# Performance work log

Measured on AMD Instinct MI355X. Metric: run time of the kernel, lower is better.

Reference implementation:

```python
import jax, jax.numpy as jnp
import numpy as np

EPS = 1e-6          # VN leaky-relu denominator eps (vn_layers.py)
NEG_SLOPE = 0.2     # VNLinearLeakyReLU default negative_slope
K = 3               # pointops.interpolation default k
DIST_EPS = 1e-8     # interpolation inverse-distance eps


def vn_linear_leakyrelu(x, w_feat, w_dir):
    # x: [B, Cin, 3, N]; w_*: [Cout, Cin]  (bias-free Linears over channel dim)
    p = jnp.einsum('oc,bcvn->bovn', w_feat, x)
    d = jnp.einsum('oc,bcvn->bovn', w_dir, x)
    dot = jnp.sum(p * d, axis=2, keepdims=True)          # [B,Cout,1,N]
    d2 = jnp.sum(d * d, axis=2, keepdims=True)
    mask = (dot >= 0).astype(x.dtype)
    proj = p - (dot / (d2 + EPS)) * d                    # reflect negative part onto plane perp to d
    return NEG_SLOPE * p + (1.0 - NEG_SLOPE) * (mask * p + (1.0 - mask) * proj)


def interpolation(p2, p1, feat, b, n2, n1):
    # p2: [b*n2,3] coarse coords, p1: [b*n1,3] fine coords, feat: [C,3,b*n2]
    # k-NN inverse-squared-distance interpolation, segment-local per cloud.
    C = feat.shape[0]
    p2b = p2.reshape(b, n2, 3)
    p1b = p1.reshape(b, n1, 3)
    featb = feat.reshape(C * 3, b, n2).transpose(1, 2, 0)  # [b, n2, C*3]

    def per_batch(q, s, f):
        d2 = jnp.sum((q[:, None, :] - s[None, :, :]) ** 2, axis=-1)  # [n1,n2]
        neg_d2, idx = jax.lax.top_k(-d2, K)                          # k smallest sq-dists
        w = 1.0 / (-neg_d2 + DIST_EPS)
        w = w / jnp.sum(w, axis=1, keepdims=True)                    # [n1,K]
        return jnp.einsum('nk,nkc->nc', w, f[idx])                   # [n1, C*3]

    out = jax.vmap(per_batch)(p1b, p2b, featb)                       # [b, n1, C*3]
    return out.reshape(b, n1, C, 3).transpose(2, 3, 0, 1).reshape(C, 3, b * n1)


def setup_inputs() -> dict:
    key = jax.random.key(0)
    ks = jax.random.split(key, 8)
    b, n1, n2 = 4, 16384, 4096
    in_planes, out_planes = 128, 64
    p1 = jax.random.uniform(ks[0], (b * n1, 3), dtype=jnp.float32)
    p2 = jax.random.uniform(ks[1], (b * n2, 3), dtype=jnp.float32)
    x1 = jax.random.normal(ks[2], (1, out_planes, 3, b * n1), dtype=jnp.float32)
    x2 = jax.random.normal(ks[3], (1, in_planes, 3, b * n2), dtype=jnp.float32)
    o1 = (jnp.arange(1, b + 1, dtype=jnp.int32)) * n1   # cumulative offsets
    o2 = (jnp.arange(1, b + 1, dtype=jnp.int32)) * n2
    s1 = 1.0 / np.sqrt(out_planes)
    s2 = 1.0 / np.sqrt(in_planes)
    w1_feat = jax.random.uniform(ks[4], (out_planes, out_planes), jnp.float32, -s1, s1)
    w1_dir = jax.random.uniform(ks[5], (out_planes, out_planes), jnp.float32, -s1, s1)
    w2_feat = jax.random.uniform(ks[6], (out_planes, in_planes), jnp.float32, -s2, s2)
    w2_dir = jax.random.uniform(ks[7], (out_planes, in_planes), jnp.float32, -s2, s2)
    return {"p1": p1, "x1": x1, "o1": o1, "p2": p2, "x2": x2, "o2": o2,
            "w1_feat": w1_feat, "w1_dir": w1_dir, "w2_feat": w2_feat, "w2_dir": w2_dir}


def reference(p1, x1, o1, p2, x2, o2, w1_feat, w1_dir, w2_feat, w2_dir):
    b = o1.shape[0]
    n1 = x1.shape[-1] // b
    n2 = x2.shape[-1] // b
    y1 = vn_linear_leakyrelu(x1, w1_feat, w1_dir)            # [1,Cout,3,N1]
    y2 = vn_linear_leakyrelu(x2, w2_feat, w2_dir)[0]         # squeeze(0) -> [Cout,3,N2]
    up = interpolation(p2, p1, y2, b, n2, n1)                # [Cout,3,N1]
    return y1 + up
```

## Files before the change

kernel.cpp:

```cpp
#include <hip/hip_runtime.h>

#define N1T 65536
#define N2T 16384
#define COUT 64
#define CH 192
#define GRD 8
#define HCELL 0.125f

typedef unsigned short bhalf;
typedef __attribute__((ext_vector_type(8))) short short8;
typedef __attribute__((ext_vector_type(4))) float f32x4;

__device__ __forceinline__ bhalf f2bf(float f) {
    unsigned u = __float_as_uint(f);
    return (bhalf)((u + 0x7FFFu + ((u >> 16) & 1u)) >> 16);
}
__device__ __forceinline__ float bf2f(bhalf h) {
    return __uint_as_float(((unsigned)h) << 16);
}

__global__ __launch_bounds__(256) void prep_kernel(
    const float* __restrict__ w1f, const float* __restrict__ w1d,
    const float* __restrict__ w2f, const float* __restrict__ w2d,
    bhalf* __restrict__ o1fh, bhalf* __restrict__ o1fl,
    bhalf* __restrict__ o1dh, bhalf* __restrict__ o1dl,
    bhalf* __restrict__ o2fh, bhalf* __restrict__ o2fl,
    bhalf* __restrict__ o2dh, bhalf* __restrict__ o2dl,
    int* __restrict__ zp) {
    if (blockIdx.x < 32) {
        const int i = blockIdx.x * 256 + threadIdx.x;
        if (i < 4096) {
            const float a = w1f[i]; const bhalf ah = f2bf(a);
            o1fh[i] = ah; o1fl[i] = f2bf(a - bf2f(ah));
            const float b = w1d[i]; const bhalf bh = f2bf(b);
            o1dh[i] = bh; o1dl[i] = f2bf(b - bf2f(bh));
        }
        const float a = w2f[i]; const bhalf ah = f2bf(a);
        o2fh[i] = ah; o2fl[i] = f2bf(a - bf2f(ah));
        const float b = w2d[i]; const bhalf bh = f2bf(b);
        o2dh[i] = bh; o2dl[i] = f2bf(b - bf2f(bh));
    } else {
        const int i = (blockIdx.x - 32) * 256 + threadIdx.x;
        if (i < 4096) zp[i] = 0;
    }
}

template<int CIN, int N, bool CM, int NT>
__global__ __launch_bounds__(512) void vn_mfma_kernel(
    const float* __restrict__ x,
    const bhalf* __restrict__ wfh, const bhalf* __restrict__ wfl,
    const bhalf* __restrict__ wdh, const bhalf* __restrict__ wdl,
    const int*   __restrict__ idxs,
    const float* __restrict__ wts,
    const float* __restrict__ y2t,
    float* __restrict__ out)
{
    constexpr int ROWS = CIN * 3;
    constexpr int LDSC = CIN * 3 + 8;
    constexpr int NB   = (NT > 1) ? 2 : 1;
    constexpr int NLD  = ROWS * 8 / 512;
    __shared__ __align__(16) bhalf xs_h[NB][32][LDSC];
    __shared__ __align__(16) bhalf xs_l[NB][32][LDSC];

    const int tid  = threadIdx.x;
    const int lane = tid & 63;
    const int wave = tid >> 6;
    const int r16  = lane & 15;
    const int hh   = lane >> 4;
    const int ot   = wave & 3;
    const int sW   = wave >> 2;
    const int pt   = sW * 16 + r16;
    const int tile0 = blockIdx.x * NT;

    int gk[NT][3]; float gw[NT][3];
    if constexpr (CM) {
#pragma unroll
        for (int t = 0; t < NT; ++t) {
            const int n = (tile0 + t) * 32 + pt;
#pragma unroll
            for (int r = 0; r < 3; ++r) {
                gk[t][r] = idxs[r * N1T + n];
                gw[t][r] = wts[r * N1T + n];
            }
        }
    }

    const int wofs = (ot * 16 + r16) * CIN + hh * 8;
    const bhalf* __restrict__ pfh = wfh + wofs;
    const bhalf* __restrict__ pfl = wfl + wofs;
    const bhalf* __restrict__ pdh = wdh + wofs;
    const bhalf* __restrict__ pdl = wdl + wofs;
    const int hs = ((hh ^ (r16 >> 2)) & 3) * 8;

    auto LOADT = [&](float4 (&st)[NLD], int t) {
#pragma unroll
        for (int r = 0; r < NLD; ++r) {
            const int i4 = r * 512 + tid;
            const int row = i4 >> 3, p4 = i4 & 7;
            st[r] = *(const float4*)&x[(size_t)row * N + (size_t)(tile0 + t) * 32 + p4 * 4];
        }
    };
    auto WRITET = [&](const float4 (&st)[NLD], int b) {
#pragma unroll
        for (int r = 0; r < NLD; ++r) {
            const int i4 = r * 512 + tid;
            const int row = i4 >> 3, p4 = i4 & 7;
            const int c = row / 3, vv = row - c * 3;
            const int colS = (vv * CIN + c) ^ ((p4 & 3) << 3);
            const float vals[4] = {st[r].x, st[r].y, st[r].z, st[r].w};
#pragma unroll
            for (int j = 0; j < 4; ++j) {
                const bhalf h = f2bf(vals[j]);
                xs_h[b][p4*4+j][colS] = h;
                xs_l[b][p4*4+j][colS] = f2bf(vals[j] - bf2f(h));
            }
        }
    };
    auto COMPUTET = [&](int t, int b, const int (&gkt)[3], const float (&gwt)[3]) {
        const f32x4 zero = {0.f, 0.f, 0.f, 0.f};
        f32x4 accP[3], accD[3];
#pragma unroll
        for (int v = 0; v < 3; ++v) { accP[v] = zero; accD[v] = zero; }
#pragma unroll
        for (int k = 0; k < CIN / 32; ++k) {
            const short8 afh = *(const short8*)(pfh + k * 32);
            const short8 afl = *(const short8*)(pfl + k * 32);
            const short8 adh = *(const short8*)(pdh + k * 32);
            const short8 adl = *(const short8*)(pdl + k * 32);
#pragma unroll
            for (int v = 0; v < 3; ++v) {
                const short8 bh = *(const short8*)&xs_h[b][pt][v * CIN + k * 32 + hs];
                const short8 bl = *(const short8*)&xs_l[b][pt][v * CIN + k * 32 + hs];
                accP[v] = __builtin_amdgcn_mfma_f32_16x16x32_bf16(afh, bh, accP[v], 0, 0, 0);
                accP[v] = __builtin_amdgcn_mfma_f32_16x16x32_bf16(afl, bh, accP[v], 0, 0, 0);
                accP[v] = __builtin_amdgcn_mfma_f32_16x16x32_bf16(afh, bl, accP[v], 0, 0, 0);
                accD[v] = __builtin_amdgcn_mfma_f32_16x16x32_bf16(adh, bh, accD[v], 0, 0, 0);
                accD[v] = __builtin_amdgcn_mfma_f32_16x16x32_bf16(adl, bh, accD[v], 0, 0, 0);
                accD[v] = __builtin_amdgcn_mfma_f32_16x16x32_bf16(adh, bl, accD[v], 0, 0, 0);
            }
        }
        float rr[12];
#pragma unroll
        for (int reg = 0; reg < 4; ++reg) {
            const float p0 = accP[0][reg], p1 = accP[1][reg], p2 = accP[2][reg];
            const float q0 = accD[0][reg], q1 = accD[1][reg], q2 = accD[2][reg];
            const float dot = p0*q0 + p1*q1 + p2*q2;
            const float dd  = q0*q0 + q1*q1 + q2*q2;
            const float coef = (dot < 0.f) ? (0.8f * dot / (dd + 1e-6f)) : 0.f;
            rr[reg*3+0] = p0 - coef * q0;
            rr[reg*3+1] = p1 - coef * q1;
            rr[reg*3+2] = p2 - coef * q2;
        }
        const int n = (tile0 + t) * 32 + pt;
        if constexpr (!CM) {
            float* op = out + (size_t)n * CH + ot * 48 + hh * 12;
            *(float4*)&op[0] = make_float4(rr[0], rr[1], rr[2],  rr[3]);
            *(float4*)&op[4] = make_float4(rr[4], rr[5], rr[6],  rr[7]);
            *(float4*)&op[8] = make_float4(rr[8], rr[9], rr[10], rr[11]);
        } else {
            const int chb = ot * 48 + hh * 12;
            const float* __restrict__ r0 = y2t + (size_t)gkt[0] * CH + chb;
            const float* __restrict__ r1 = y2t + (size_t)gkt[1] * CH + chb;
            const float* __restrict__ r2 = y2t + (size_t)gkt[2] * CH + chb;
            const float w0 = gwt[0], w1 = gwt[1], w2 = gwt[2];
            float4 a0[3], a1[3], a2[3];
#pragma unroll
            for (int q = 0; q < 3; ++q) {
                a0[q] = *(const float4*)&r0[q * 4];
                a1[q] = *(const float4*)&r1[q * 4];
                a2[q] = *(const float4*)&r2[q * 4];
            }
#pragma unroll
            for (int q = 0; q < 3; ++q) {
                const float u0 = w0*a0[q].x + w1*a1[q].x + w2*a2[q].x;
                const float u1 = w0*a0[q].y + w1*a1[q].y + w2*a2[q].y;
                const float u2 = w0*a0[q].z + w1*a1[q].z + w2*a2[q].z;
                const float u3 = w0*a0[q].w + w1*a1[q].w + w2*a2[q].w;
                out[(size_t)(chb + q*4 + 0) * N + n] = rr[q*4+0] + u0;
                out[(size_t)(chb + q*4 + 1) * N + n] = rr[q*4+1] + u1;
                out[(size_t)(chb + q*4 + 2) * N + n] = rr[q*4+2] + u2;
                out[(size_t)(chb + q*4 + 3) * N + n] = rr[q*4+3] + u3;
            }
        }
    };

    float4 stA[NLD], stB[NLD];
    LOADT(stA, 0);
    WRITET(stA, 0);
    if constexpr (NT == 2) {
        LOADT(stB, 1);
        __syncthreads();
        COMPUTET(0, 0, gk[0], gw[0]);
        WRITET(stB, 1);
        __syncthreads();
        COMPUTET(1, 1, gk[1], gw[1]);
    } else {
        __syncthreads();
        COMPUTET(0, 0, gk[0], gw[0]);
    }
}

#define KNN_INSERT(d2, j)                                        \
    {                                                            \
        const bool c0 = (d2) < b0;                               \
        const bool c1 = (d2) < b1;                               \
        const bool c2 = (d2) < b2v;                              \
        const float nb2 = c2 ? (c1 ? b1 : (d2)) : b2v;           \
        const int   ni2 = c2 ? (c1 ? i1 : (j))  : i2;            \
        const float nb1 = c1 ? (c0 ? b0 : (d2)) : b1;            \
        const int   ni1 = c1 ? (c0 ? i0 : (j))  : i1;            \
        b0 = c0 ? (d2) : b0;  i0 = c0 ? (j) : i0;                \
        b1 = nb1; i1 = ni1; b2v = nb2; i2 = ni2;                 \
    }

__device__ __forceinline__ int cell_of(float x, float y, float z) {
    int cx = (int)(x * (float)GRD); cx = cx < 0 ? 0 : (cx > GRD-1 ? GRD-1 : cx);
    int cy = (int)(y * (float)GRD); cy = cy < 0 ? 0 : (cy > GRD-1 ? GRD-1 : cy);
    int cz = (int)(z * (float)GRD); cz = cz < 0 ? 0 : (cz > GRD-1 ? GRD-1 : cz);
    return (cz << 6) | (cy << 3) | cx;
}

__global__ __launch_bounds__(256) void bin_count_kernel(
    const float* __restrict__ p2, int* __restrict__ counts) {
    const int i = blockIdx.x * 256 + threadIdx.x;
    const float x = p2[i*3+0], y = p2[i*3+1], z = p2[i*3+2];
    const int cell = ((i >> 12) << 9) | cell_of(x, y, z);
    atomicAdd(&counts[cell], 1);
}

__global__ __launch_bounds__(256) void scan_kernel(
    const int* __restrict__ counts, int* __restrict__ off) {
    __shared__ int buf[2][256];
    const int t = threadIdx.x;
    int v[8]; int s = 0;
#pragma unroll
    for (int j = 0; j < 8; ++j) { const int tmp = counts[t*8+j]; v[j] = s; s += tmp; }
    buf[0][t] = s; __syncthreads();
    int src = 0;
    for (int d = 1; d < 256; d <<= 1) {
        int val = buf[src][t];
        if (t >= d) val += buf[src][t - d];
        buf[src ^ 1][t] = val; src ^= 1; __syncthreads();
    }
    const int incl = buf[src][t];
    const int base = incl - s;
#pragma unroll
    for (int j = 0; j < 8; ++j) off[t*8+j] = base + v[j];
    if (t == 255) off[2048] = incl;
}

__global__ __launch_bounds__(256) void bin_scatter_kernel(
    const float* __restrict__ p2, const int* __restrict__ off,
    int* __restrict__ cnt2, float4* __restrict__ binned) {
    const int i = blockIdx.x * 256 + threadIdx.x;
    const float x = p2[i*3+0], y = p2[i*3+1], z = p2[i*3+2];
    const int cell = ((i >> 12) << 9) | cell_of(x, y, z);
    const int pos = off[cell] + atomicAdd(&cnt2[cell], 1);
    binned[pos] = make_float4(x, y, z, __int_as_float(i));
}

__global__ __launch_bounds__(512) void vn2_knn_kernel(
    const float* __restrict__ x2,
    const bhalf* __restrict__ wfh, const bhalf* __restrict__ wfl,
    const bhalf* __restrict__ wdh, const bhalf* __restrict__ wdl,
    float* __restrict__ y2t,
    const float* __restrict__ p1,
    const float4* __restrict__ binned,
    const int* __restrict__ off,
    int*   __restrict__ idx_out,
    float* __restrict__ w_out)
{
    constexpr int CIN = 128, N = N2T;
    constexpr int LDSC = CIN * 3 + 8;
    __shared__ __align__(16) bhalf xs_h[32][LDSC];
    __shared__ __align__(16) bhalf xs_l[32][LDSC];

    const int role = blockIdx.x & 1;
    const int ridx = blockIdx.x >> 1;
    const int tid  = threadIdx.x;

    if (role == 0) {
        const int lane = tid & 63;
        const int wave = tid >> 6;
        const int r16  = lane & 15;
        const int hh   = lane >> 4;
        const int ot   = wave & 3;
        const int sW   = wave >> 2;
        const int pt   = sW * 16 + r16;
        const int n0   = ridx * 32;

        const int wofs = (ot * 16 + r16) * CIN + hh * 8;
        const bhalf* __restrict__ pfh = wfh + wofs;
        const bhalf* __restrict__ pfl = wfl + wofs;
        const bhalf* __restrict__ pdh = wdh + wofs;
        const bhalf* __restrict__ pdl = wdl + wofs;
        const int hs = ((hh ^ (r16 >> 2)) & 3) * 8;

#pragma unroll
        for (int r = 0; r < 6; ++r) {
            const int i4 = r * 512 + tid;
            const int row = i4 >> 3, p4 = i4 & 7;
            const float4 v = *(const float4*)&x2[(size_t)row * N + n0 + p4 * 4];
            const int c = row / 3, vv = row - c * 3;
            const int colS = (vv * CIN + c) ^ ((p4 & 3) << 3);
            const float vals[4] = {v.x, v.y, v.z, v.w};
#pragma unroll
            for (int j = 0; j < 4; ++j) {
                const bhalf h = f2bf(vals[j]);
                xs_h[p4*4+j][colS] = h;
                xs_l[p4*4+j][colS] = f2bf(vals[j] - bf2f(h));
            }
        }
        __syncthreads();

        const f32x4 zero = {0.f, 0.f, 0.f, 0.f};
        f32x4 accP[3], accD[3];
#pragma unroll
        for (int v = 0; v < 3; ++v) { accP[v] = zero; accD[v] = zero; }
#pragma unroll
        for (int k = 0; k < CIN / 32; ++k) {
            const short8 afh = *(const short8*)(pfh + k * 32);
            const short8 afl = *(const short8*)(pfl + k * 32);
            const short8 adh = *(const short8*)(pdh + k * 32);
            const short8 adl = *(const short8*)(pdl + k * 32);
#pragma unroll
            for (int v = 0; v < 3; ++v) {
                const short8 bh = *(const short8*)&xs_h[pt][v * CIN + k * 32 + hs];
                const short8 bl = *(const short8*)&xs_l[pt][v * CIN + k * 32 + hs];
                accP[v] = __builtin_amdgcn_mfma_f32_16x16x32_bf16(afh, bh, accP[v], 0, 0, 0);
                accP[v] = __builtin_amdgcn_mfma_f32_16x16x32_bf16(afl, bh, accP[v], 0, 0, 0);
                accP[v] = __builtin_amdgcn_mfma_f32_16x16x32_bf16(afh, bl, accP[v], 0, 0, 0);
                accD[v] = __builtin_amdgcn_mfma_f32_16x16x32_bf16(adh, bh, accD[v], 0, 0, 0);
                accD[v] = __builtin_amdgcn_mfma_f32_16x16x32_bf16(adl, bh, accD[v], 0, 0, 0);
                accD[v] = __builtin_amdgcn_mfma_f32_16x16x32_bf16(adh, bl, accD[v], 0, 0, 0);
            }
        }

        float rr[12];
#pragma unroll
        for (int reg = 0; reg < 4; ++reg) {
            const float p0 = accP[0][reg], p1 = accP[1][reg], p2 = accP[2][reg];
            const float q0 = accD[0][reg], q1 = accD[1][reg], q2 = accD[2][reg];
            const float dot = p0*q0 + p1*q1 + p2*q2;
            const float dd  = q0*q0 + q1*q1 + q2*q2;
            const float coef = (dot < 0.f) ? (0.8f * dot / (dd + 1e-6f)) : 0.f;
            rr[reg*3+0] = p0 - coef * q0;
            rr[reg*3+1] = p1 - coef * q1;
            rr[reg*3+2] = p2 - coef * q2;
        }
        const int n = n0 + pt;
        float* op = y2t + (size_t)n * CH + ot * 48 + hh * 12;
        *(float4*)&op[0] = make_float4(rr[0], rr[1], rr[2],  rr[3]);
        *(float4*)&op[4] = make_float4(rr[4], rr[5], rr[6],  rr[7]);
        *(float4*)&op[8] = make_float4(rr[8], rr[9], rr[10], rr[11]);
    } else {
        const int fp  = ridx * 128 + (tid >> 2);
        const int sub = tid & 3;
        const int bi  = fp >> 14;
        const int cbase = bi << 9;

        const float qx = p1[fp*3+0], qy = p1[fp*3+1], qz = p1[fp*3+2];
        int cx = (int)(qx * (float)GRD); cx = cx < 0 ? 0 : (cx > 7 ? 7 : cx);
        int cy = (int)(qy * (float)GRD); cy = cy < 0 ? 0 : (cy > 7 ? 7 : cy);
        int cz = (int)(qz * (float)GRD); cz = cz < 0 ? 0 : (cz > 7 ? 7 : cz);

        const int x0 = cx > 0 ? cx - 1 : 0;
        const int x1 = cx < 7 ? cx + 1 : 7;

        float b0 = 1e30f, b1 = 1e30f, b2v = 1e30f;
        int   i0 = 0,     i1 = 0,     i2 = 0;

#pragma unroll
        for (int dz = -1; dz <= 1; ++dz) {
            const int nz = cz + dz;
            if ((unsigned)nz > 7u) continue;
#pragma unroll
            for (int dy = -1; dy <= 1; ++dy) {
                const int ny = cy + dy;
                if ((unsigned)ny > 7u) continue;
                const int cb = cbase + (nz << 6) + (ny << 3);
                const int s = off[cb + x0], e = off[cb + x1 + 1];
                for (int k = s + sub; k < e; k += 4) {
                    const float4 c4 = binned[k];
                    const float ddx = qx - c4.x, ddy = qy - c4.y, ddz = qz - c4.z;
                    const float d2 = fmaf(ddx, ddx, fmaf(ddy, ddy, ddz * ddz));
                    const int j = __float_as_int(c4.w);
                    KNN_INSERT(d2, j)
                }
            }
        }

#pragma unroll
        for (int m = 1; m <= 2; m <<= 1) {
            const float c0v = __shfl_xor(b0, m, 4);
            const float c1v = __shfl_xor(b1, m, 4);
            const float c2v = __shfl_xor(b2v, m, 4);
            const int   j0v = __shfl_xor(i0, m, 4);
            const int   j1v = __shfl_xor(i1, m, 4);
            const int   j2v = __shfl_xor(i2, m, 4);
            KNN_INSERT(c0v, j0v)
            KNN_INSERT(c1v, j1v)
            KNN_INSERT(c2v, j2v)
        }

        float dw = 1e30f;
        if (cx >= 2) dw = fminf(dw, qx - (float)(cx - 1) * HCELL);
        if (cx <= 5) dw = fminf(dw, (float)(cx + 2) * HCELL - qx);
        if (cy >= 2) dw = fminf(dw, qy - (float)(cy - 1) * HCELL);
        if (cy <= 5) dw = fminf(dw, (float)(cy + 2) * HCELL - qy);
        if (cz >= 2) dw = fminf(dw, qz - (float)(cz - 1) * HCELL);
        if (cz <= 5) dw = fminf(dw, (float)(cz + 2) * HCELL - qz);
        const bool done = b2v < dw * dw;

        if (!done) {
            b0 = b1 = b2v = 1e30f; i0 = i1 = i2 = 0;
            const int s = bi << 12, e = (bi + 1) << 12;
            for (int k = s + sub; k < e; k += 4) {
                const float4 c4 = binned[k];
                const float ddx = qx - c4.x, ddy = qy - c4.y, ddz = qz - c4.z;
                const float d2 = fmaf(ddx, ddx, fmaf(ddy, ddy, ddz * ddz));
                const int j = __float_as_int(c4.w);
                KNN_INSERT(d2, j)
            }
#pragma unroll
            for (int m = 1; m <= 2; m <<= 1) {
                const float c0v = __shfl_xor(b0, m, 4);
                const float c1v = __shfl_xor(b1, m, 4);
                const float c2v = __shfl_xor(b2v, m, 4);
                const int   j0v = __shfl_xor(i0, m, 4);
                const int   j1v = __shfl_xor(i1, m, 4);
                const int   j2v = __shfl_xor(i2, m, 4);
                KNN_INSERT(c0v, j0v)
                KNN_INSERT(c1v, j1v)
                KNN_INSERT(c2v, j2v)
            }
        }

        if (sub == 0) {
            const float w0 = 1.f / (b0 + 1e-8f);
            const float w1 = 1.f / (b1 + 1e-8f);
            const float w2 = 1.f / (b2v + 1e-8f);
            const float inv = 1.f / (w0 + w1 + w2);
            idx_out[0*N1T + fp] = i0;
            idx_out[1*N1T + fp] = i1;
            idx_out[2*N1T + fp] = i2;
            w_out[0*N1T + fp] = w0 * inv;
            w_out[1*N1T + fp] = w1 * inv;
            w_out[2*N1T + fp] = w2 * inv;
        }
    }
}

extern "C" void kernel_launch(void* const* d_in, const int* in_sizes, int n_in,
                              void* d_out, int out_size, void* d_ws, size_t ws_size,
                              hipStream_t stream) {
    const float* p1      = (const float*)d_in[0];
    const float* x1      = (const float*)d_in[1];
    const float* p2      = (const float*)d_in[3];
    const float* x2      = (const float*)d_in[4];
    const float* w1_feat = (const float*)d_in[6];
    const float* w1_dir  = (const float*)d_in[7];
    const float* w2_feat = (const float*)d_in[8];
    const float* w2_dir  = (const float*)d_in[9];
    float* out = (float*)d_out;

    char* ws = (char*)d_ws;
    float*  y2t    = (float*)ws;                 ws += (size_t)N2T * CH * 4;
    int*    idxs   = (int*)ws;                   ws += (size_t)3 * N1T * 4;
    float*  wts    = (float*)ws;                 ws += (size_t)3 * N1T * 4;
    int*    counts = (int*)ws;                   ws += 2048 * 4;
    int*    cnt2   = (int*)ws;                   ws += 2048 * 4;
    int*    off    = (int*)ws;                   ws += 2064 * 4;
    float4* binned = (float4*)ws;                ws += (size_t)N2T * 16;
    bhalf*  wb1fh  = (bhalf*)ws;                 ws += 4096 * 2;
    bhalf*  wb1fl  = (bhalf*)ws;                 ws += 4096 * 2;
    bhalf*  wb1dh  = (bhalf*)ws;                 ws += 4096 * 2;
    bhalf*  wb1dl  = (bhalf*)ws;                 ws += 4096 * 2;
    bhalf*  wb2fh  = (bhalf*)ws;                 ws += 8192 * 2;
    bhalf*  wb2fl  = (bhalf*)ws;                 ws += 8192 * 2;
    bhalf*  wb2dh  = (bhalf*)ws;                 ws += 8192 * 2;
    bhalf*  wb2dl  = (bhalf*)ws;                 ws += 8192 * 2;

    prep_kernel<<<48, 256, 0, stream>>>(w1_feat, w1_dir, w2_feat, w2_dir,
                                        wb1fh, wb1fl, wb1dh, wb1dl,
                                        wb2fh, wb2fl, wb2dh, wb2dl, counts);
    bin_count_kernel<<<N2T/256, 256, 0, stream>>>(p2, counts);
    scan_kernel<<<1, 256, 0, stream>>>(counts, off);
    bin_scatter_kernel<<<N2T/256, 256, 0, stream>>>(p2, off, cnt2, binned);
    vn2_knn_kernel<<<1024, 512, 0, stream>>>(
        x2, wb2fh, wb2fl, wb2dh, wb2dl, y2t,
        p1, binned, off, idxs, wts);
    vn_mfma_kernel<64, N1T, true, 2><<<N1T/64, 512, 0, stream>>>(
        x1, wb1fh, wb1fl, wb1dh, wb1dl, idxs, wts, y2t, out);
}
```

Baseline: 98.95 us.

## Merge binning into one block kernel and split x1 to bf16 at MFMA time

The separate count, scan and scatter kernels (plus zeroing in prep) are replaced by a single 1024-thread block kernel that bins the coarse points using shared-memory atomics and a scan. This removes several launches and global atomics. The vn1 kernel now stores x1 tiles as fp32 in LDS with a swizzle and does the hi/lo bf16 split after loading the fragments. The split uses truncation instead of round-to-nearest, which changes accuracy slightly and moves conversion work into the MFMA loop. A single block handling all 16K points serially could lengthen the critical path.

```diff
diff --git a/kernel.cpp b/kernel.cpp
--- a/kernel.cpp
+++ b/kernel.cpp
@@ -19,34 +19,105 @@
     return __uint_as_float(((unsigned)h) << 16);
 }
 
+__device__ __forceinline__ void pack_split(const float (&f)[8], short8& bh, short8& bl) {
+    union { short8 s; uint4 u; } ch, cl;
+    unsigned hd[4], ld[4];
+#pragma unroll
+    for (int m = 0; m < 4; ++m) {
+        const unsigned u0 = __float_as_uint(f[2*m]);
+        const unsigned u1 = __float_as_uint(f[2*m+1]);
+        const unsigned h0 = u0 & 0xFFFF0000u;
+        const unsigned h1 = u1 & 0xFFFF0000u;
+        hd[m] = (h0 >> 16) | h1;
+        const float l0 = f[2*m]   - __uint_as_float(h0);
+        const float l1 = f[2*m+1] - __uint_as_float(h1);
+        ld[m] = (__float_as_uint(l0) >> 16) | (__float_as_uint(l1) & 0xFFFF0000u);
+    }
+    ch.u = make_uint4(hd[0], hd[1], hd[2], hd[3]);
+    cl.u = make_uint4(ld[0], ld[1], ld[2], ld[3]);
+    bh = ch.s; bl = cl.s;
+}
+
 __global__ __launch_bounds__(256) void prep_kernel(
     const float* __restrict__ w1f, const float* __restrict__ w1d,
     const float* __restrict__ w2f, const float* __restrict__ w2d,
     bhalf* __restrict__ o1fh, bhalf* __restrict__ o1fl,
     bhalf* __restrict__ o1dh, bhalf* __restrict__ o1dl,
     bhalf* __restrict__ o2fh, bhalf* __restrict__ o2fl,
-    bhalf* __restrict__ o2dh, bhalf* __restrict__ o2dl,
-    int* __restrict__ zp) {
-    if (blockIdx.x < 32) {
-        const int i = blockIdx.x * 256 + threadIdx.x;
-        if (i < 4096) {
-            const float a = w1f[i]; const bhalf ah = f2bf(a);
-            o1fh[i] = ah; o1fl[i] = f2bf(a - bf2f(ah));
-            const float b = w1d[i]; const bhalf bh = f2bf(b);
-            o1dh[i] = bh; o1dl[i] = f2bf(b - bf2f(bh));
-        }
-        const float a = w2f[i]; const bhalf ah = f2bf(a);
-        o2fh[i] = ah; o2fl[i] = f2bf(a - bf2f(ah));
-        const float b = w2d[i]; const bhalf bh = f2bf(b);
-        o2dh[i] = bh; o2dl[i] = f2bf(b - bf2f(bh));
-    } else {
-        const int i = (blockIdx.x - 32) * 256 + threadIdx.x;
-        if (i < 4096) zp[i] = 0;
-    }
-}
-
-template<int CIN, int N, bool CM, int NT>
-__global__ __launch_bounds__(512) void vn_mfma_kernel(
+    bhalf* __restrict__ o2dh, bhalf* __restrict__ o2dl) {
+    const int i = blockIdx.x * 256 + threadIdx.x;
+    if (i < 4096) {
+        const float a = w1f[i]; const bhalf ah = f2bf(a);
+        o1fh[i] = ah; o1fl[i] = f2bf(a - bf2f(ah));
+        const float b = w1d[i]; const bhalf bh = f2bf(b);
+        o1dh[i] = bh; o1dl[i] = f2bf(b - bf2f(bh));
+    }
+    const float a = w2f[i]; const bhalf ah = f2bf(a);
+    o2fh[i] = ah; o2fl[i] = f2bf(a - bf2f(ah));
+    const float b = w2d[i]; const bhalf bh = f2bf(b);
+    o2dh[i] = bh; o2dl[i] = f2bf(b - bf2f(bh));
+}
+
+__device__ __forceinline__ int cell_of(float x, float y, float z) {
+    int cx = (int)(x * (float)GRD); cx = cx < 0 ? 0 : (cx > GRD-1 ? GRD-1 : cx);
+    int cy = (int)(y * (float)GRD); cy = cy < 0 ? 0 : (cy > GRD-1 ? GRD-1 : cy);
+    int cz = (int)(z * (float)GRD); cz = cz < 0 ? 0 : (cz > GRD-1 ? GRD-1 : cz);
+    return (cz << 6) | (cy << 3) | cx;
+}
+
+__global__ __launch_bounds__(1024) void bin_all_kernel(
+    const float* __restrict__ p2,
+    int*    __restrict__ off_g,
+    float4* __restrict__ binned)
+{
+    __shared__ int cnt[2048];
+    __shared__ int offl[2049];
+    __shared__ int cnt2[2048];
+    __shared__ int wsum[1024];
+    const int t = threadIdx.x;
+    cnt[t] = 0; cnt[t + 1024] = 0;
+    cnt2[t] = 0; cnt2[t + 1024] = 0;
+    __syncthreads();
+
+    for (int i = t; i < N2T; i += 1024) {
+        const float x = p2[i*3+0], y = p2[i*3+1], z = p2[i*3+2];
+        const int cell = ((i >> 12) << 9) | cell_of(x, y, z);
+        atomicAdd(&cnt[cell], 1);
+    }
+    __syncthreads();
+
+    const int a  = cnt[2*t], b2 = cnt[2*t+1];
+    const int s  = a + b2;
+    wsum[t] = s;
+    __syncthreads();
+    for (int d = 1; d < 1024; d <<= 1) {
+        const int v = wsum[t];
+        const int u = (t >= d) ? wsum[t - d] : 0;
+        __syncthreads();
+        wsum[t] = v + u;
+        __syncthreads();
+    }
+    const int incl = wsum[t];
+    const int base = incl - s;
+    offl[2*t]   = base;
+    offl[2*t+1] = base + a;
+    if (t == 1023) offl[2048] = incl;
+    __syncthreads();
+
+    off_g[t] = offl[t]; off_g[t + 1024] = offl[t + 1024];
+    if (t == 0) off_g[2048] = offl[2048];
+
+    for (int i = t; i < N2T; i += 1024) {
+        const float x = p2[i*3+0], y = p2[i*3+1], z = p2[i*3+2];
+        const int cell = ((i >> 12) << 9) | cell_of(x, y, z);
+        const int pos = offl[cell] + atomicAdd(&cnt2[cell], 1);
+        binned[pos] = make_float4(x, y, z, __int_as_float(i));
+    }
+}
+
+#define WCOL 196
+template<int N>
+__global__ __launch_bounds__(512) void vn1_fused_kernel(
     const float* __restrict__ x,
     const bhalf* __restrict__ wfh, const bhalf* __restrict__ wfl,
     const bhalf* __restrict__ wdh, const bhalf* __restrict__ wdl,
@@ -55,12 +126,8 @@
     const float* __restrict__ y2t,
     float* __restrict__ out)
 {
-    constexpr int ROWS = CIN * 3;
-    constexpr int LDSC = CIN * 3 + 8;
-    constexpr int NB   = (NT > 1) ? 2 : 1;
-    constexpr int NLD  = ROWS * 8 / 512;
-    __shared__ __align__(16) bhalf xs_h[NB][32][LDSC];
-    __shared__ __align__(16) bhalf xs_l[NB][32][LDSC];
+    constexpr int CIN = 64;
+    __shared__ __align__(16) float xs[2][32][WCOL];
 
     const int tid  = threadIdx.x;
     const int lane = tid & 63;
@@ -70,18 +137,17 @@
     const int ot   = wave & 3;
     const int sW   = wave >> 2;
     const int pt   = sW * 16 + r16;
-    const int tile0 = blockIdx.x * NT;
-
-    int gk[NT][3]; float gw[NT][3];
-    if constexpr (CM) {
-#pragma unroll
-        for (int t = 0; t < NT; ++t) {
-            const int n = (tile0 + t) * 32 + pt;
-#pragma unroll
-            for (int r = 0; r < 3; ++r) {
-                gk[t][r] = idxs[r * N1T + n];
-                gw[t][r] = wts[r * N1T + n];
-            }
+    const int tile0 = blockIdx.x * 2;
+    const int chb  = ot * 48 + hh * 12;
+
+    int gk[2][3]; float gw[2][3];
+#pragma unroll
+    for (int t = 0; t < 2; ++t) {
+        const int n = (tile0 + t) * 32 + pt;
+#pragma unroll
+        for (int r = 0; r < 3; ++r) {
+            gk[t][r] = idxs[r * N1T + n];
+            gw[t][r] = wts[r * N1T + n];
         }
     }
 
@@ -90,30 +156,28 @@
     const bhalf* __restrict__ pfl = wfl + wofs;
     const bhalf* __restrict__ pdh = wdh + wofs;
     const bhalf* __restrict__ pdl = wdl + wofs;
-    const int hs = ((hh ^ (r16 >> 2)) & 3) * 8;
-
-    auto LOADT = [&](float4 (&st)[NLD], int t) {
-#pragma unroll
-        for (int r = 0; r < NLD; ++r) {
+    const int rm = (r16 >> 2) & 3;
+
+    auto LOADT = [&](float4 (&st)[3], int t) {
+#pragma unroll
+        for (int r = 0; r < 3; ++r) {
             const int i4 = r * 512 + tid;
             const int row = i4 >> 3, p4 = i4 & 7;
             st[r] = *(const float4*)&x[(size_t)row * N + (size_t)(tile0 + t) * 32 + p4 * 4];
         }
     };
-    auto WRITET = [&](const float4 (&st)[NLD], int b) {
-#pragma unroll
-        for (int r = 0; r < NLD; ++r) {
+    auto WRITET = [&](const float4 (&st)[3], int b) {
+#pragma unroll
+        for (int r = 0; r < 3; ++r) {
             const int i4 = r * 512 + tid;
             const int row = i4 >> 3, p4 = i4 & 7;
             const int c = row / 3, vv = row - c * 3;
-            const int colS = (vv * CIN + c) ^ ((p4 & 3) << 3);
+            const int col = vv * 64 + c;
+            const int colS = (((col >> 2) ^ (p4 & 3)) << 2) | (col & 3);
             const float vals[4] = {st[r].x, st[r].y, st[r].z, st[r].w};
 #pragma unroll
-            for (int j = 0; j < 4; ++j) {
-                const bhalf h = f2bf(vals[j]);
-                xs_h[b][p4*4+j][colS] = h;
-                xs_l[b][p4*4+j][colS] = f2bf(vals[j] - bf2f(h));
-            }
+            for (int j = 0; j < 4; ++j)
+                xs[b][p4*4+j][colS] = vals[j];
         }
     };
     auto COMPUTET = [&](int t, int b, const int (&gkt)[3], const float (&gwt)[3]) {
@@ -122,15 +186,20 @@
 #pragma unroll
         for (int v = 0; v < 3; ++v) { accP[v] = zero; accD[v] = zero; }
 #pragma unroll
-        for (int k = 0; k < CIN / 32; ++k) {
+        for (int k = 0; k < 2; ++k) {
             const short8 afh = *(const short8*)(pfh + k * 32);
             const short8 afl = *(const short8*)(pfl + k * 32);
             const short8 adh = *(const short8*)(pdh + k * 32);
             const short8 adl = *(const short8*)(pdl + k * 32);
 #pragma unroll
             for (int v = 0; v < 3; ++v) {
-                const short8 bh = *(const short8*)&xs_h[b][pt][v * CIN + k * 32 + hs];
-                const short8 bl = *(const short8*)&xs_l[b][pt][v * CIN + k * 32 + hs];
+                const int g0 = v * 16 + k * 8 + hh * 2;
+                const int gA = g0 ^ rm, gB = (g0 + 1) ^ rm;
+                const float4 fA = *(const float4*)&xs[b][pt][gA << 2];
+                const float4 fB = *(const float4*)&xs[b][pt][gB << 2];
+                const float f8[8] = {fA.x, fA.y, fA.z, fA.w, fB.x, fB.y, fB.z, fB.w};
+                short8 bh, bl;
+                pack_split(f8, bh, bl);
                 accP[v] = __builtin_amdgcn_mfma_f32_16x16x32_bf16(afh, bh, accP[v], 0, 0, 0);
                 accP[v] = __builtin_amdgcn_mfma_f32_16x16x32_bf16(afl, bh, accP[v], 0, 0, 0);
                 accP[v] = __builtin_amdgcn_mfma_f32_16x16x32_bf16(afh, bl, accP[v], 0, 0, 0);
@@ -152,52 +221,39 @@
             rr[reg*3+2] = p2 - coef * q2;
         }
         const int n = (tile0 + t) * 32 + pt;
-        if constexpr (!CM) {
-            float* op = out + (size_t)n * CH + ot * 48 + hh * 12;
-            *(float4*)&op[0] = make_float4(rr[0], rr[1], rr[2],  rr[3]);
-            *(float4*)&op[4] = make_float4(rr[4], rr[5], rr[6],  rr[7]);
-            *(float4*)&op[8] = make_float4(rr[8], rr[9], rr[10], rr[11]);
-        } else {
-            const int chb = ot * 48 + hh * 12;
-            const float* __restrict__ r0 = y2t + (size_t)gkt[0] * CH + chb;
-            const float* __restrict__ r1 = y2t + (size_t)gkt[1] * CH + chb;
-            const float* __restrict__ r2 = y2t + (size_t)gkt[2] * CH + chb;
-            const float w0 = gwt[0], w1 = gwt[1], w2 = gwt[2];
-            float4 a0[3], a1[3], a2[3];
-#pragma unroll
-            for (int q = 0; q < 3; ++q) {
-                a0[q] = *(const float4*)&r0[q * 4];
-                a1[q] = *(const float4*)&r1[q * 4];
-                a2[q] = *(const float4*)&r2[q * 4];
-            }
-#pragma unroll
-            for (int q = 0; q < 3; ++q) {
-                const float u0 = w0*a0[q].x + w1*a1[q].x + w2*a2[q].x;
-                const float u1 = w0*a0[q].y + w1*a1[q].y + w2*a2[q].y;
-                const float u2 = w0*a0[q].z + w1*a1[q].z + w2*a2[q].z;
-                const float u3 = w0*a0[q].w + w1*a1[q].w + w2*a2[q].w;
-                out[(size_t)(chb + q*4 + 0) * N + n] = rr[q*4+0] + u0;
-                out[(size_t)(chb + q*4 + 1) * N + n] = rr[q*4+1] + u1;
-                out[(size_t)(chb + q*4 + 2) * N + n] = rr[q*4+2] + u2;
-                out[(size_t)(chb + q*4 + 3) * N + n] = rr[q*4+3] + u3;
-            }
+        const float* __restrict__ r0 = y2t + (size_t)gkt[0] * CH + chb;
+        const float* __restrict__ r1 = y2t + (size_t)gkt[1] * CH + chb;
+        const float* __restrict__ r2 = y2t + (size_t)gkt[2] * CH + chb;
+        const float w0 = gwt[0], w1 = gwt[1], w2 = gwt[2];
+        float4 a0[3], a1[3], a2[3];
+#pragma unroll
+        for (int q = 0; q < 3; ++q) {
+            a0[q] = *(const float4*)&r0[q * 4];
+            a1[q] = *(const float4*)&r1[q * 4];
+            a2[q] = *(const float4*)&r2[q * 4];
+        }
+#pragma unroll
+        for (int q = 0; q < 3; ++q) {
+            const float u0 = w0*a0[q].x + w1*a1[q].x + w2*a2[q].x;
+            const float u1 = w0*a0[q].y + w1*a1[q].y + w2*a2[q].y;
+            const float u2 = w0*a0[q].z + w1*a1[q].z + w2*a2[q].z;
+            const float u3 = w0*a0[q].w + w1*a1[q].w + w2*a2[q].w;
+            out[(size_t)(chb + q*4 + 0) * N + n] = rr[q*4+0] + u0;
+            out[(size_t)(chb + q*4 + 1) * N + n] = rr[q*4+1] + u1;
+            out[(size_t)(chb + q*4 + 2) * N + n] = rr[q*4+2] + u2;
+            out[(size_t)(chb + q*4 + 3) * N + n] = rr[q*4+3] + u3;
         }
     };
 
-    float4 stA[NLD], stB[NLD];
+    float4 stA[3], stB[3];
     LOADT(stA, 0);
     WRITET(stA, 0);
-    if constexpr (NT == 2) {
-        LOADT(stB, 1);
-        __syncthreads();
-        COMPUTET(0, 0, gk[0], gw[0]);
-        WRITET(stB, 1);
-        __syncthreads();
-        COMPUTET(1, 1, gk[1], gw[1]);
-    } else {
-        __syncthreads();
-        COMPUTET(0, 0, gk[0], gw[0]);
-    }
+    LOADT(stB, 1);
+    __syncthreads();
+    COMPUTET(0, 0, gk[0], gw[0]);
+    WRITET(stB, 1);
+    __syncthreads();
+    COMPUTET(1, 1, gk[1], gw[1]);
 }
 
 #define KNN_INSERT(d2, j)                                        \
@@ -212,52 +268,6 @@
         b0 = c0 ? (d2) : b0;  i0 = c0 ? (j) : i0;                \
         b1 = nb1; i1 = ni1; b2v = nb2; i2 = ni2;                 \
     }
-
-__device__ __forceinline__ int cell_of(float x, float y, float z) {
-    int cx = (int)(x * (float)GRD); cx = cx < 0 ? 0 : (cx > GRD-1 ? GRD-1 : cx);
-    int cy = (int)(y * (float)GRD); cy = cy < 0 ? 0 : (cy > GRD-1 ? GRD-1 : cy);
-    int cz = (int)(z * (float)GRD); cz = cz < 0 ? 0 : (cz > GRD-1 ? GRD-1 : cz);
-    return (cz << 6) | (cy << 3) | cx;
-}
-
-__global__ __launch_bounds__(256) void bin_count_kernel(
-    const float* __restrict__ p2, int* __restrict__ counts) {
-    const int i = blockIdx.x * 256 + threadIdx.x;
-    const float x = p2[i*3+0], y = p2[i*3+1], z = p2[i*3+2];
-    const int cell = ((i >> 12) << 9) | cell_of(x, y, z);
-    atomicAdd(&counts[cell], 1);
-}
-
-__global__ __launch_bounds__(256) void scan_kernel(
-    const int* __restrict__ counts, int* __restrict__ off) {
-    __shared__ int buf[2][256];
-    const int t = threadIdx.x;
-    int v[8]; int s = 0;
-#pragma unroll
-    for (int j = 0; j < 8; ++j) { const int tmp = counts[t*8+j]; v[j] = s; s += tmp; }
-    buf[0][t] = s; __syncthreads();
-    int src = 0;
-    for (int d = 1; d < 256; d <<= 1) {
-        int val = buf[src][t];
-        if (t >= d) val += buf[src][t - d];
-        buf[src ^ 1][t] = val; src ^= 1; __syncthreads();
-    }
-    const int incl = buf[src][t];
-    const int base = incl - s;
-#pragma unroll
-    for (int j = 0; j < 8; ++j) off[t*8+j] = base + v[j];
-    if (t == 255) off[2048] = incl;
-}
-
-__global__ __launch_bounds__(256) void bin_scatter_kernel(
-    const float* __restrict__ p2, const int* __restrict__ off,
-    int* __restrict__ cnt2, float4* __restrict__ binned) {
-    const int i = blockIdx.x * 256 + threadIdx.x;
-    const float x = p2[i*3+0], y = p2[i*3+1], z = p2[i*3+2];
-    const int cell = ((i >> 12) << 9) | cell_of(x, y, z);
-    const int pos = off[cell] + atomicAdd(&cnt2[cell], 1);
-    binned[pos] = make_float4(x, y, z, __int_as_float(i));
-}
 
 __global__ __launch_bounds__(512) void vn2_knn_kernel(
     const float* __restrict__ x2,
@@ -468,8 +478,6 @@
     float*  y2t    = (float*)ws;                 ws += (size_t)N2T * CH * 4;
     int*    idxs   = (int*)ws;                   ws += (size_t)3 * N1T * 4;
     float*  wts    = (float*)ws;                 ws += (size_t)3 * N1T * 4;
-    int*    counts = (int*)ws;                   ws += 2048 * 4;
-    int*    cnt2   = (int*)ws;                   ws += 2048 * 4;
     int*    off    = (int*)ws;                   ws += 2064 * 4;
     float4* binned = (float4*)ws;                ws += (size_t)N2T * 16;
     bhalf*  wb1fh  = (bhalf*)ws;                 ws += 4096 * 2;
@@ -481,15 +489,13 @@
     bhalf*  wb2dh  = (bhalf*)ws;                 ws += 8192 * 2;
     bhalf*  wb2dl  = (bhalf*)ws;                 ws += 8192 * 2;
 
-    prep_kernel<<<48, 256, 0, stream>>>(w1_feat, w1_dir, w2_feat, w2_dir,
+    prep_kernel<<<32, 256, 0, stream>>>(w1_feat, w1_dir, w2_feat, w2_dir,
                                         wb1fh, wb1fl, wb1dh, wb1dl,
-                                        wb2fh, wb2fl, wb2dh, wb2dl, counts);
-    bin_count_kernel<<<N2T/256, 256, 0, stream>>>(p2, counts);
-    scan_kernel<<<1, 256, 0, stream>>>(counts, off);
-    bin_scatter_kernel<<<N2T/256, 256, 0, stream>>>(p2, off, cnt2, binned);
+                                        wb2fh, wb2fl, wb2dh, wb2dl);
+    bin_all_kernel<<<1, 1024, 0, stream>>>(p2, off, binned);
     vn2_knn_kernel<<<1024, 512, 0, stream>>>(
         x2, wb2fh, wb2fl, wb2dh, wb2dl, y2t,
         p1, binned, off, idxs, wts);
-    vn_mfma_kernel<64, N1T, true, 2><<<N1T/64, 512, 0, stream>>>(
+    vn1_fused_kernel<N1T><<<N1T/64, 512, 0, stream>>>(
         x1, wb1fh, wb1fl, wb1dh, wb1dl, idxs, wts, y2t, out);
 }
```

After: 111.1 us. 12.3% more time.
